# Kernel tuning notes

Hardware: AMD Instinct MI355X
Metric: run time of the kernel (lower is better)

The kernel has to match this reference:

```python
import jax, jax.numpy as jnp
import numpy as np

B, T, IN, H = 32, 256, 64, 128
TOP_K = 5
TRUNC = 100   # truncate_length: detach h,c every TRUNC steps
EPS = 1e-7
NEG = -1e9


def setup_inputs() -> dict:
    key = jax.random.key(0)
    ks = jax.random.split(key, 6)
    s = 1.0 / np.sqrt(H)  # torch LSTMCell default init bound
    xav = float(1.414 * np.sqrt(6.0 / (2 * H + 1)))  # xavier_uniform gain=1.414
    return {
        "x": jax.random.normal(ks[0], (B, T, IN), jnp.float32),
        "W_ih": jax.random.uniform(ks[1], (4 * H, IN), jnp.float32, -s, s),
        "W_hh": jax.random.uniform(ks[2], (4 * H, H), jnp.float32, -s, s),
        "b_ih": jax.random.uniform(ks[3], (4 * H,), jnp.float32, -s, s),
        "b_hh": jax.random.uniform(ks[4], (4 * H,), jnp.float32, -s, s),
        "w_t": jax.random.uniform(ks[5], (2 * H, 1), jnp.float32, -xav, xav),
    }


def _lstm_cell(x_t, h, c, W_ih, W_hh, b_ih, b_hh):
    # torch gate order: i, f, g, o
    g = x_t @ W_ih.T + h @ W_hh.T + (b_ih + b_hh)
    i, f, gg, o = jnp.split(g, 4, axis=-1)
    c = jax.nn.sigmoid(f) * c + jax.nn.sigmoid(i) * jnp.tanh(gg)
    h = jax.nn.sigmoid(o) * jnp.tanh(c)
    return h, c


def reference(x, W_ih, W_hh, b_ih, b_hh, w_t):
    Bv, Tv, _ = x.shape
    Hh = W_hh.shape[1]
    # score = w_t . tanh(cat(h_t, h_old)) splits additively since tanh is elementwise
    w_a = w_t[:Hh, 0]
    w_b = w_t[Hh:, 0]
    pos = jnp.arange(Tv + 1)

    def step(carry, inp):
        h, c, h_old = carry          # h_old: [B, T+1, H], slot 0 = initial zeros
        i, x_t = inp
        det = ((i + 1) % TRUNC) == 0
        h = jnp.where(det, jax.lax.stop_gradient(h), h)
        c = jnp.where(det, jax.lax.stop_gradient(c), c)
        h, c = _lstm_cell(x_t, h, c, W_ih, W_hh, b_ih, b_hh)
        rem = i + 1                  # remember_size
        mask = pos < rem             # [T+1] valid memory slots
        # attention scores over stored states
        s = (jnp.tanh(h) @ w_a)[:, None] + jnp.tanh(h_old) @ w_b  # [B, T+1]
        s_valid = jnp.where(mask[None, :], s, NEG)
        delta = jax.lax.top_k(s_valid, TOP_K)[0][:, -1] + EPS
        w_sp = jnp.clip(s_valid - delta[:, None], 0.0)
        w_sp = w_sp / (w_sp.sum(axis=1, keepdims=True) + EPS)
        # Sparse_attention returns raw scores when remember_size <= top_k
        attn_w = jnp.where(rem <= TOP_K, s, w_sp)
        attn_c = jnp.einsum('bt,bth->bh', jnp.where(mask[None, :], attn_w, 0.0), h_old)
        h = h + attn_c
        h_old = jax.lax.dynamic_update_slice(h_old, h[:, None, :], (0, rem, 0))
        return (h, c, h_old), (attn_c, attn_w)

    h0 = jnp.zeros((Bv, Hh), x.dtype)
    c0 = jnp.zeros((Bv, Hh), x.dtype)
    buf0 = jnp.zeros((Bv, Tv + 1, Hh), x.dtype)
    xs = (jnp.arange(Tv), jnp.swapaxes(x, 0, 1))
    _, (attn_c_all, attn_w_all) = jax.lax.scan(step, (h0, c0, buf0), xs)
    # module returns last step's (attn_c, out_attn_w); final remember_size == T
    return attn_c_all[-1], attn_w_all[-1][:, :Tv, None]
```

## Files before the change

kernel.cpp:

```cpp
#include <hip/hip_runtime.h>
#include <math.h>

#define NEGF -1000000000.0f
#define EPSF 1e-7f


typedef float v4f __attribute__((ext_vector_type(4)));
#define FMA4(a, b, c) __builtin_elementwise_fma((a), (b), (c))

#define RAWBAR() asm volatile("s_waitcnt lgkmcnt(0)\n\ts_barrier" ::: "memory")

__device__ __forceinline__ float fsigmoid(float x) {
  return 1.0f / (1.0f + __expf(-x));
}
__device__ __forceinline__ float ftanh(float x) {
  return 1.0f - 2.0f / (1.0f + __expf(2.0f * x));
}

__device__ __forceinline__ float wave_allsum(float v) {
#if __has_builtin(__builtin_amdgcn_update_dpp) && __has_builtin(__builtin_amdgcn_readlane)
  float f = v;
#define DPPSTEP(ctrl, rmask) { \
    int t = __builtin_amdgcn_update_dpp(0, __builtin_bit_cast(int, f), \
                                        ctrl, rmask, 0xf, true); \
    f += __builtin_bit_cast(float, t); }
  DPPSTEP(0x111, 0xf)
  DPPSTEP(0x112, 0xf)
  DPPSTEP(0x114, 0xf)
  DPPSTEP(0x118, 0xf)
  DPPSTEP(0x142, 0xa)
  DPPSTEP(0x143, 0x8)
#undef DPPSTEP
  return __builtin_bit_cast(float,
      __builtin_amdgcn_readlane(__builtin_bit_cast(int, f), 63));
#else
  for (int off = 1; off < 64; off <<= 1) v += __shfl_xor(v, off, 64);
  return v;
#endif
}

__global__ __launch_bounds__(512) void xw_kernel(
    const float* __restrict__ x, const float* __restrict__ W_ih,
    const float* __restrict__ b_ih, const float* __restrict__ b_hh,
    float* __restrict__ xw)
{
  const int t0 = blockIdx.x * 32;
  const int b  = blockIdx.y;
  const int g  = threadIdx.x;

  __shared__ float sx[32 * 64];
  ((float4*)sx)[threadIdx.x] =
      ((const float4*)(x + (size_t)(b * 256 + t0) * 64))[threadIdx.x];

  const float4* wr = (const float4*)(W_ih + (size_t)g * 64);
  float4 w0 = wr[0],  w1 = wr[1],  w2 = wr[2],  w3 = wr[3],
         w4 = wr[4],  w5 = wr[5],  w6 = wr[6],  w7 = wr[7],
         w8 = wr[8],  w9 = wr[9],  w10 = wr[10], w11 = wr[11],
         w12 = wr[12], w13 = wr[13], w14 = wr[14], w15 = wr[15];
  const float bias = b_ih[g] + b_hh[g];
  __syncthreads();

  float* dst = xw + (size_t)(b * 256 + t0) * 512 + g;
  for (int tt = 0; tt < 32; ++tt) {
    const float4* xr = (const float4*)(sx + tt * 64);
    float a0 = 0.0f, a1 = 0.0f, a2 = 0.0f, a3 = 0.0f;
#define XSTEP(j) { float4 hv = xr[j]; \
    a0 = fmaf(w##j.x, hv.x, a0); a1 = fmaf(w##j.y, hv.y, a1); \
    a2 = fmaf(w##j.z, hv.z, a2); a3 = fmaf(w##j.w, hv.w, a3); }
    XSTEP(0) XSTEP(1) XSTEP(2) XSTEP(3) XSTEP(4) XSTEP(5) XSTEP(6) XSTEP(7)
    XSTEP(8) XSTEP(9) XSTEP(10) XSTEP(11) XSTEP(12) XSTEP(13) XSTEP(14) XSTEP(15)
#undef XSTEP
    dst[(size_t)tt * 512] = (a0 + a1) + (a2 + a3) + bias;
  }
}

__global__
__attribute__((amdgpu_flat_work_group_size(512, 512), amdgpu_waves_per_eu(2, 2)))
void lstm_attn(
    const float* __restrict__ xw, const float* __restrict__ W_hh,
    const float* __restrict__ w_t, float* __restrict__ out)
{
  const int b   = blockIdx.x;
  const int tid = threadIdx.x;
  const int l   = tid & 63;
  const int wid = tid >> 6;
  const int g2  = tid & 255;
  const int q   = tid >> 8;

  __shared__ float ho[257 * 128];
  __shared__ float sh_part[2 * 512];
  __shared__ float sh_d[8];
  __shared__ float sh_pa[2];
  __shared__ float sh_dn[2];

  const v4f* pA = (const v4f*)(W_hh + (size_t)g2 * 128 + (q << 6));
  const v4f* pB = (const v4f*)(W_hh + (size_t)(g2 + 256) * 128 + (q << 6));
  v4f wA0 = pA[0],  wA1 = pA[1],  wA2 = pA[2],  wA3 = pA[3],
      wA4 = pA[4],  wA5 = pA[5],  wA6 = pA[6],  wA7 = pA[7],
      wA8 = pA[8],  wA9 = pA[9],  wA10 = pA[10], wA11 = pA[11],
      wA12 = pA[12], wA13 = pA[13], wA14 = pA[14], wA15 = pA[15];
  v4f wB0 = pB[0],  wB1 = pB[1],  wB2 = pB[2],  wB3 = pB[3],
      wB4 = pB[4],  wB5 = pB[5],  wB6 = pB[6],  wB7 = pB[7],
      wB8 = pB[8],  wB9 = pB[9],  wB10 = pB[10], wB11 = pB[11],
      wB12 = pB[12], wB13 = pB[13], wB14 = pB[14], wB15 = pB[15];

  const int j = (wid << 6) + l;
  float cc = 0.0f;
  float wa = 0.0f, wb = 0.0f;
  float t5v0 = 0.0f, t5v1 = NEGF, t5v2 = NEGF, t5v3 = NEGF, t5v4 = NEGF;
  int   t5i0 = 0, t5i1 = 0, t5i2 = 0, t5i3 = 0;
  float gn0 = 0.0f, gn1 = 0.0f, gn2 = 0.0f, gn3 = 0.0f;
  int   ofs0 = 0, ofs1 = 0, ofs2 = 0, ofs3 = 0;

  if (wid < 2) {
    wa = w_t[j]; wb = w_t[128 + j];
    ho[j] = 0.0f;
    __builtin_amdgcn_s_setprio(1);
  }
  if (tid == 0) sh_d[0] = 0.0f;
  __syncthreads();

  const float* xwb = xw + (size_t)b * 256 * 512;
  float xcA = 0.0f, xcB = 0.0f;
  if (q == 0) { xcA = xwb[g2]; xcB = xwb[g2 + 256]; }

  for (int i = 0; i < 256; ++i) {
    const int rem = i + 1;

    v4f aA = {xcA, 0.0f, 0.0f, 0.0f};
    v4f aB = {xcB, 0.0f, 0.0f, 0.0f};
    if (q == 0 && i < 255) {
      const float* xn = xwb + (size_t)(i + 1) * 512;
      xcA = xn[g2]; xcB = xn[g2 + 256];
    }
    const v4f* hh4 = (const v4f*)(ho + i * 128 + (q << 6));
#define KS(k) { v4f hv = hh4[k]; \
    aA = FMA4(wA##k, hv, aA); aB = FMA4(wB##k, hv, aB); }
    KS(0) KS(1) KS(2) KS(3) KS(4) KS(5) KS(6) KS(7)
    KS(8) KS(9) KS(10) KS(11) KS(12) KS(13) KS(14) KS(15)
#undef KS
    {
      float* sp = sh_part + (q << 9) + g2;
      sp[0]   = (aA.x + aA.y) + (aA.z + aA.w);
      sp[256] = (aB.x + aB.y) + (aB.z + aB.w);
    }

    float hv0 = 0.0f, hv1 = 0.0f, hv2 = 0.0f, hv3 = 0.0f;
    if (wid < 2 && i >= 5) {
      hv0 = ho[ofs0]; hv1 = ho[ofs1]; hv2 = ho[ofs2]; hv3 = ho[ofs3];
    }
    RAWBAR();

    float hc = 0.0f, at = 0.0f;
    if (wid < 2) {
      const float* s0 = sh_part + j;
      float Pi = s0[0]   + s0[512];
      float Pf = s0[128] + s0[640];
      float Pg = s0[256] + s0[768];
      float Po = s0[384] + s0[896];
      cc = fsigmoid(Pf) * cc + fsigmoid(Pi) * ftanh(Pg);
      hc = fsigmoid(Po) * ftanh(cc);
    }
    if (i < 5) {
      if (wid < 2) {
        float pa = wave_allsum(ftanh(hc) * wa);
        if (l == 0) sh_pa[wid] = pa;
      }
      RAWBAR();
      if (wid < 2) {
        float a = sh_pa[0] + sh_pa[1];
        at = 0.0f;
        for (int t = 0; t <= i; ++t)
          at = fmaf(a + sh_d[t], ho[t * 128 + j], at);
      }
    } else if (wid < 2) {
      at = gn0 * hv0;
      at = fmaf(gn1, hv1, at);
      at = fmaf(gn2, hv2, at);
      at = fmaf(gn3, hv3, at);
    }
    if (wid < 2) {
      float hn = hc + at;
      ho[rem * 128 + j] = hn;
      float pdn = wave_allsum(ftanh(hn) * wb);
      if (l == 0) sh_dn[wid] = pdn;
      if (i == 255) {
        out[b * 128 + j] = at;
        if (wid == 0) {
          #pragma unroll
          for (int m = 0; m < 4; ++m) {
            int t = l + 64 * m;
            float val = 0.0f;
            if (t == t5i0) val = gn0;
            if (t == t5i1) val = gn1;
            if (t == t5i2) val = gn2;
            if (t == t5i3) val = gn3;
            out[4096 + b * 256 + t] = val;
          }
        }
      }
    }
    RAWBAR();

    if (wid < 2 && i < 255) {
      float dn = sh_dn[0] + sh_dn[1];
      if (wid == 0 && l == 0 && i < 4) sh_d[rem] = dn;
      float v = dn; int vi = rem;
      if (v > t5v0) { float tv = t5v0; int ti = t5i0; t5v0 = v; t5i0 = vi; v = tv; vi = ti; }
      if (v > t5v1) { float tv = t5v1; int ti = t5i1; t5v1 = v; t5i1 = vi; v = tv; vi = ti; }
      if (v > t5v2) { float tv = t5v2; int ti = t5i2; t5v2 = v; t5i2 = vi; v = tv; vi = ti; }
      if (v > t5v3) { float tv = t5v3; int ti = t5i3; t5v3 = v; t5i3 = vi; v = tv; vi = ti; }
      if (v > t5v4) { t5v4 = v; }
      float g0 = fmaxf(t5v0 - t5v4 - EPSF, 0.0f);
      float g1 = fmaxf(t5v1 - t5v4 - EPSF, 0.0f);
      float g2f = fmaxf(t5v2 - t5v4 - EPSF, 0.0f);
      float g3 = fmaxf(t5v3 - t5v4 - EPSF, 0.0f);
      float inv = 1.0f / (((g0 + g1) + (g2f + g3)) + EPSF);
      gn0 = g0 * inv; gn1 = g1 * inv; gn2 = g2f * inv; gn3 = g3 * inv;
      ofs0 = (t5i0 << 7) + j; ofs1 = (t5i1 << 7) + j;
      ofs2 = (t5i2 << 7) + j; ofs3 = (t5i3 << 7) + j;
    }
  }
}

extern "C" void kernel_launch(void* const* d_in, const int* in_sizes, int n_in,
                              void* d_out, int out_size, void* d_ws, size_t ws_size,
                              hipStream_t stream) {
  const float* x    = (const float*)d_in[0];
  const float* W_ih = (const float*)d_in[1];
  const float* W_hh = (const float*)d_in[2];
  const float* b_ih = (const float*)d_in[3];
  const float* b_hh = (const float*)d_in[4];
  const float* w_t  = (const float*)d_in[5];
  float* out = (float*)d_out;

  float* xw = (float*)d_ws;

  xw_kernel<<<dim3(8, 32), 512, 0, stream>>>(x, W_ih, b_ih, b_hh, xw);
  lstm_attn<<<dim3(32), 512, 0, stream>>>(xw, W_hh, w_t, out);
}
```

Baseline: 368.1 us.

## Replicate LSTM cell update in every wave to drop a barrier per step

Each of the 8 waves now computes the full 128-wide gate and attention update redundantly, two hidden units per lane, and writes its own private copy of h. This removes the second block barrier per timestep and the cross-wave partial-sum exchange through shared memory. Top-k hidden states are kept in registers instead of a 257-step shared-memory history, and the gate partials are double-buffered so a single barrier per step suffices. The cost is redundant transcendental math in all waves and more register pressure, and the wave priority boost is dropped.

```diff
diff --git a/kernel.cpp b/kernel.cpp
--- a/kernel.cpp
+++ b/kernel.cpp
@@ -87,11 +87,10 @@
   const int g2  = tid & 255;
   const int q   = tid >> 8;
 
-  __shared__ float ho[257 * 128];
-  __shared__ float sh_part[2 * 512];
+  __shared__ float hpriv[8][128];
+  __shared__ float sh_part[2][1024];
+  __shared__ float ho5[5 * 128];
   __shared__ float sh_d[8];
-  __shared__ float sh_pa[2];
-  __shared__ float sh_dn[2];
 
   const v4f* pA = (const v4f*)(W_hh + (size_t)g2 * 128 + (q << 6));
   const v4f* pB = (const v4f*)(W_hh + (size_t)(g2 + 256) * 128 + (q << 6));
@@ -104,19 +103,18 @@
       wB8 = pB[8],  wB9 = pB[9],  wB10 = pB[10], wB11 = pB[11],
       wB12 = pB[12], wB13 = pB[13], wB14 = pB[14], wB15 = pB[15];
 
-  const int j = (wid << 6) + l;
-  float cc = 0.0f;
-  float wa = 0.0f, wb = 0.0f;
+  const int j0 = 2 * l, j1 = 2 * l + 1;
+  float cc0 = 0.0f, cc1 = 0.0f;
+  const float wa0 = w_t[j0], wa1 = w_t[j1];
+  const float wb0 = w_t[128 + j0], wb1 = w_t[128 + j1];
   float t5v0 = 0.0f, t5v1 = NEGF, t5v2 = NEGF, t5v3 = NEGF, t5v4 = NEGF;
   int   t5i0 = 0, t5i1 = 0, t5i2 = 0, t5i3 = 0;
+  float h5a0 = 0.0f, h5a1 = 0.0f, h5a2 = 0.0f, h5a3 = 0.0f;
+  float h5b0 = 0.0f, h5b1 = 0.0f, h5b2 = 0.0f, h5b3 = 0.0f;
   float gn0 = 0.0f, gn1 = 0.0f, gn2 = 0.0f, gn3 = 0.0f;
-  int   ofs0 = 0, ofs1 = 0, ofs2 = 0, ofs3 = 0;
-
-  if (wid < 2) {
-    wa = w_t[j]; wb = w_t[128 + j];
-    ho[j] = 0.0f;
-    __builtin_amdgcn_s_setprio(1);
-  }
+
+  *(float2*)(&hpriv[wid][j0]) = make_float2(0.0f, 0.0f);
+  if (wid == 0) *(float2*)(ho5 + j0) = make_float2(0.0f, 0.0f);
   if (tid == 0) sh_d[0] = 0.0f;
   __syncthreads();
 
@@ -133,83 +131,91 @@
       const float* xn = xwb + (size_t)(i + 1) * 512;
       xcA = xn[g2]; xcB = xn[g2 + 256];
     }
-    const v4f* hh4 = (const v4f*)(ho + i * 128 + (q << 6));
+    const v4f* hh4 = (const v4f*)(&hpriv[wid][q << 6]);
 #define KS(k) { v4f hv = hh4[k]; \
     aA = FMA4(wA##k, hv, aA); aB = FMA4(wB##k, hv, aB); }
     KS(0) KS(1) KS(2) KS(3) KS(4) KS(5) KS(6) KS(7)
     KS(8) KS(9) KS(10) KS(11) KS(12) KS(13) KS(14) KS(15)
 #undef KS
     {
-      float* sp = sh_part + (q << 9) + g2;
+      float* sp = sh_part[i & 1] + (q << 9) + g2;
       sp[0]   = (aA.x + aA.y) + (aA.z + aA.w);
       sp[256] = (aB.x + aB.y) + (aB.z + aB.w);
     }
-
-    float hv0 = 0.0f, hv1 = 0.0f, hv2 = 0.0f, hv3 = 0.0f;
-    if (wid < 2 && i >= 5) {
-      hv0 = ho[ofs0]; hv1 = ho[ofs1]; hv2 = ho[ofs2]; hv3 = ho[ofs3];
-    }
     RAWBAR();
 
-    float hc = 0.0f, at = 0.0f;
-    if (wid < 2) {
-      const float* s0 = sh_part + j;
-      float Pi = s0[0]   + s0[512];
-      float Pf = s0[128] + s0[640];
-      float Pg = s0[256] + s0[768];
-      float Po = s0[384] + s0[896];
-      cc = fsigmoid(Pf) * cc + fsigmoid(Pi) * ftanh(Pg);
-      hc = fsigmoid(Po) * ftanh(cc);
-    }
-    if (i < 5) {
-      if (wid < 2) {
-        float pa = wave_allsum(ftanh(hc) * wa);
-        if (l == 0) sh_pa[wid] = pa;
+    const float* s0 = sh_part[i & 1];
+    float2 Pi0 = *(const float2*)(s0 + j0);
+    float2 Pi1 = *(const float2*)(s0 + 512 + j0);
+    float2 Pf0 = *(const float2*)(s0 + 128 + j0);
+    float2 Pf1 = *(const float2*)(s0 + 640 + j0);
+    float2 Pg0 = *(const float2*)(s0 + 256 + j0);
+    float2 Pg1 = *(const float2*)(s0 + 768 + j0);
+    float2 Po0 = *(const float2*)(s0 + 384 + j0);
+    float2 Po1 = *(const float2*)(s0 + 896 + j0);
+    float Pi_x = Pi0.x + Pi1.x, Pi_y = Pi0.y + Pi1.y;
+    float Pf_x = Pf0.x + Pf1.x, Pf_y = Pf0.y + Pf1.y;
+    float Pg_x = Pg0.x + Pg1.x, Pg_y = Pg0.y + Pg1.y;
+    float Po_x = Po0.x + Po1.x, Po_y = Po0.y + Po1.y;
+    cc0 = fsigmoid(Pf_x) * cc0 + fsigmoid(Pi_x) * ftanh(Pg_x);
+    cc1 = fsigmoid(Pf_y) * cc1 + fsigmoid(Pi_y) * ftanh(Pg_y);
+    float hc0 = fsigmoid(Po_x) * ftanh(cc0);
+    float hc1 = fsigmoid(Po_y) * ftanh(cc1);
+
+    float at0, at1;
+    if (i >= 5) {
+      at0 = gn0 * h5a0;            at1 = gn0 * h5b0;
+      at0 = fmaf(gn1, h5a1, at0);  at1 = fmaf(gn1, h5b1, at1);
+      at0 = fmaf(gn2, h5a2, at0);  at1 = fmaf(gn2, h5b2, at1);
+      at0 = fmaf(gn3, h5a3, at0);  at1 = fmaf(gn3, h5b3, at1);
+    } else {
+      float a = wave_allsum(ftanh(hc0) * wa0 + ftanh(hc1) * wa1);
+      at0 = 0.0f; at1 = 0.0f;
+      for (int t = 0; t <= i; ++t) {
+        float s = a + sh_d[t];
+        float2 hv = *(const float2*)(ho5 + t * 128 + j0);
+        at0 = fmaf(s, hv.x, at0);
+        at1 = fmaf(s, hv.y, at1);
       }
-      RAWBAR();
-      if (wid < 2) {
-        float a = sh_pa[0] + sh_pa[1];
-        at = 0.0f;
-        for (int t = 0; t <= i; ++t)
-          at = fmaf(a + sh_d[t], ho[t * 128 + j], at);
+    }
+    float hn0 = hc0 + at0, hn1 = hc1 + at1;
+    *(float2*)(&hpriv[wid][j0]) = make_float2(hn0, hn1);
+    if (wid == 0 && rem <= 4)
+      *(float2*)(ho5 + rem * 128 + j0) = make_float2(hn0, hn1);
+    if (i == 255 && wid == 0) {
+      out[b * 128 + j0] = at0; out[b * 128 + j1] = at1;
+      #pragma unroll
+      for (int m = 0; m < 4; ++m) {
+        int t = l + 64 * m;
+        float val = 0.0f;
+        if (t == t5i0) val = gn0;
+        if (t == t5i1) val = gn1;
+        if (t == t5i2) val = gn2;
+        if (t == t5i3) val = gn3;
+        out[4096 + b * 256 + t] = val;
       }
-    } else if (wid < 2) {
-      at = gn0 * hv0;
-      at = fmaf(gn1, hv1, at);
-      at = fmaf(gn2, hv2, at);
-      at = fmaf(gn3, hv3, at);
-    }
-    if (wid < 2) {
-      float hn = hc + at;
-      ho[rem * 128 + j] = hn;
-      float pdn = wave_allsum(ftanh(hn) * wb);
-      if (l == 0) sh_dn[wid] = pdn;
-      if (i == 255) {
-        out[b * 128 + j] = at;
-        if (wid == 0) {
-          #pragma unroll
-          for (int m = 0; m < 4; ++m) {
-            int t = l + 64 * m;
-            float val = 0.0f;
-            if (t == t5i0) val = gn0;
-            if (t == t5i1) val = gn1;
-            if (t == t5i2) val = gn2;
-            if (t == t5i3) val = gn3;
-            out[4096 + b * 256 + t] = val;
-          }
-        }
-      }
-    }
-    RAWBAR();
-
-    if (wid < 2 && i < 255) {
-      float dn = sh_dn[0] + sh_dn[1];
+    }
+
+    if (i < 255) {
+      float dn = wave_allsum(ftanh(hn0) * wb0 + ftanh(hn1) * wb1);
       if (wid == 0 && l == 0 && i < 4) sh_d[rem] = dn;
-      float v = dn; int vi = rem;
-      if (v > t5v0) { float tv = t5v0; int ti = t5i0; t5v0 = v; t5i0 = vi; v = tv; vi = ti; }
-      if (v > t5v1) { float tv = t5v1; int ti = t5i1; t5v1 = v; t5i1 = vi; v = tv; vi = ti; }
-      if (v > t5v2) { float tv = t5v2; int ti = t5i2; t5v2 = v; t5i2 = vi; v = tv; vi = ti; }
-      if (v > t5v3) { float tv = t5v3; int ti = t5i3; t5v3 = v; t5i3 = vi; v = tv; vi = ti; }
+      float v = dn; int vi = rem; float va = hn0, vb = hn1;
+      if (v > t5v0) { float tv = t5v0; t5v0 = v; v = tv;
+                      int   ti = t5i0; t5i0 = vi; vi = ti;
+                      float ta = h5a0; h5a0 = va; va = ta;
+                      float tb = h5b0; h5b0 = vb; vb = tb; }
+      if (v > t5v1) { float tv = t5v1; t5v1 = v; v = tv;
+                      int   ti = t5i1; t5i1 = vi; vi = ti;
+                      float ta = h5a1; h5a1 = va; va = ta;
+                      float tb = h5b1; h5b1 = vb; vb = tb; }
+      if (v > t5v2) { float tv = t5v2; t5v2 = v; v = tv;
+                      int   ti = t5i2; t5i2 = vi; vi = ti;
+                      float ta = h5a2; h5a2 = va; va = ta;
+                      float tb = h5b2; h5b2 = vb; vb = tb; }
+      if (v > t5v3) { float tv = t5v3; t5v3 = v; v = tv;
+                      int   ti = t5i3; t5i3 = vi; vi = ti;
+                      float ta = h5a3; h5a3 = va; va = ta;
+                      float tb = h5b3; h5b3 = vb; vb = tb; }
       if (v > t5v4) { t5v4 = v; }
       float g0 = fmaxf(t5v0 - t5v4 - EPSF, 0.0f);
       float g1 = fmaxf(t5v1 - t5v4 - EPSF, 0.0f);
@@ -217,8 +223,6 @@
       float g3 = fmaxf(t5v3 - t5v4 - EPSF, 0.0f);
       float inv = 1.0f / (((g0 + g1) + (g2f + g3)) + EPSF);
       gn0 = g0 * inv; gn1 = g1 * inv; gn2 = g2f * inv; gn3 = g3 * inv;
-      ofs0 = (t5i0 << 7) + j; ofs1 = (t5i1 << 7) + j;
-      ofs2 = (t5i2 << 7) + j; ofs3 = (t5i3 << 7) + j;
     }
   }
 }
```

Result: slower. 526.1 us (+42.9%).

## Add two dedicated cell/attention waves separate from matvec waves

Applied to the files above, without the earlier changes.

Grows the recurrent block from 512 to 640 threads. The 8 original waves now only compute the W_hh matvec partials. Two extra waves (wid>=8) handle the LSTM cell update, the attention, the top-k tracking and the output writes. This splits the serial cell and attention work off the waves that hold the weight registers, aiming to relieve register pressure and scheduling contention. In exchange it adds more waves per CU and more threads taking part in every barrier. The 640-thread waves also load the weight registers they no longer use.

```diff
diff --git a/kernel.cpp b/kernel.cpp
--- a/kernel.cpp
+++ b/kernel.cpp
@@ -75,7 +75,7 @@
 }
 
 __global__
-__attribute__((amdgpu_flat_work_group_size(512, 512), amdgpu_waves_per_eu(2, 2)))
+__attribute__((amdgpu_flat_work_group_size(640, 640), amdgpu_waves_per_eu(2)))
 void lstm_attn(
     const float* __restrict__ xw, const float* __restrict__ W_hh,
     const float* __restrict__ w_t, float* __restrict__ out)
@@ -85,7 +85,8 @@
   const int l   = tid & 63;
   const int wid = tid >> 6;
   const int g2  = tid & 255;
-  const int q   = tid >> 8;
+  const int q   = (tid >> 8) & 1;
+  const int cw  = wid - 8;
 
   __shared__ float ho[257 * 128];
   __shared__ float sh_part[2 * 512];
@@ -104,7 +105,7 @@
       wB8 = pB[8],  wB9 = pB[9],  wB10 = pB[10], wB11 = pB[11],
       wB12 = pB[12], wB13 = pB[13], wB14 = pB[14], wB15 = pB[15];
 
-  const int j = (wid << 6) + l;
+  const int j = (cw << 6) + l;
   float cc = 0.0f;
   float wa = 0.0f, wb = 0.0f;
   float t5v0 = 0.0f, t5v1 = NEGF, t5v2 = NEGF, t5v3 = NEGF, t5v4 = NEGF;
@@ -112,7 +113,7 @@
   float gn0 = 0.0f, gn1 = 0.0f, gn2 = 0.0f, gn3 = 0.0f;
   int   ofs0 = 0, ofs1 = 0, ofs2 = 0, ofs3 = 0;
 
-  if (wid < 2) {
+  if (wid >= 8) {
     wa = w_t[j]; wb = w_t[128 + j];
     ho[j] = 0.0f;
     __builtin_amdgcn_s_setprio(1);
@@ -122,37 +123,37 @@
 
   const float* xwb = xw + (size_t)b * 256 * 512;
   float xcA = 0.0f, xcB = 0.0f;
-  if (q == 0) { xcA = xwb[g2]; xcB = xwb[g2 + 256]; }
+  if (wid < 8 && q == 0 && wid < 4) { xcA = xwb[g2]; xcB = xwb[g2 + 256]; }
 
   for (int i = 0; i < 256; ++i) {
     const int rem = i + 1;
 
-    v4f aA = {xcA, 0.0f, 0.0f, 0.0f};
-    v4f aB = {xcB, 0.0f, 0.0f, 0.0f};
-    if (q == 0 && i < 255) {
-      const float* xn = xwb + (size_t)(i + 1) * 512;
-      xcA = xn[g2]; xcB = xn[g2 + 256];
-    }
-    const v4f* hh4 = (const v4f*)(ho + i * 128 + (q << 6));
+    if (wid < 8) {
+      v4f aA = {xcA, 0.0f, 0.0f, 0.0f};
+      v4f aB = {xcB, 0.0f, 0.0f, 0.0f};
+      if (wid < 4 && i < 255) {
+        const float* xn = xwb + (size_t)(i + 1) * 512;
+        xcA = xn[g2]; xcB = xn[g2 + 256];
+      }
+      const v4f* hh4 = (const v4f*)(ho + i * 128 + (q << 6));
 #define KS(k) { v4f hv = hh4[k]; \
-    aA = FMA4(wA##k, hv, aA); aB = FMA4(wB##k, hv, aB); }
-    KS(0) KS(1) KS(2) KS(3) KS(4) KS(5) KS(6) KS(7)
-    KS(8) KS(9) KS(10) KS(11) KS(12) KS(13) KS(14) KS(15)
+      aA = FMA4(wA##k, hv, aA); aB = FMA4(wB##k, hv, aB); }
+      KS(0) KS(1) KS(2) KS(3) KS(4) KS(5) KS(6) KS(7)
+      KS(8) KS(9) KS(10) KS(11) KS(12) KS(13) KS(14) KS(15)
 #undef KS
-    {
       float* sp = sh_part + (q << 9) + g2;
       sp[0]   = (aA.x + aA.y) + (aA.z + aA.w);
       sp[256] = (aB.x + aB.y) + (aB.z + aB.w);
     }
 
     float hv0 = 0.0f, hv1 = 0.0f, hv2 = 0.0f, hv3 = 0.0f;
-    if (wid < 2 && i >= 5) {
+    if (wid >= 8 && i >= 5) {
       hv0 = ho[ofs0]; hv1 = ho[ofs1]; hv2 = ho[ofs2]; hv3 = ho[ofs3];
     }
     RAWBAR();
 
     float hc = 0.0f, at = 0.0f;
-    if (wid < 2) {
+    if (wid >= 8) {
       const float* s0 = sh_part + j;
       float Pi = s0[0]   + s0[512];
       float Pf = s0[128] + s0[640];
@@ -162,31 +163,32 @@
       hc = fsigmoid(Po) * ftanh(cc);
     }
     if (i < 5) {
-      if (wid < 2) {
+      if (wid >= 8) {
         float pa = wave_allsum(ftanh(hc) * wa);
-        if (l == 0) sh_pa[wid] = pa;
+        if (l == 0) sh_pa[cw] = pa;
       }
       RAWBAR();
-      if (wid < 2) {
+      if (wid >= 8) {
         float a = sh_pa[0] + sh_pa[1];
         at = 0.0f;
         for (int t = 0; t <= i; ++t)
           at = fmaf(a + sh_d[t], ho[t * 128 + j], at);
       }
-    } else if (wid < 2) {
+    } else if (wid >= 8) {
       at = gn0 * hv0;
       at = fmaf(gn1, hv1, at);
       at = fmaf(gn2, hv2, at);
       at = fmaf(gn3, hv3, at);
     }
-    if (wid < 2) {
-      float hn = hc + at;
+    float hn = 0.0f;
+    if (wid >= 8) {
+      hn = hc + at;
       ho[rem * 128 + j] = hn;
       float pdn = wave_allsum(ftanh(hn) * wb);
-      if (l == 0) sh_dn[wid] = pdn;
+      if (l == 0) sh_dn[cw] = pdn;
       if (i == 255) {
         out[b * 128 + j] = at;
-        if (wid == 0) {
+        if (cw == 0) {
           #pragma unroll
           for (int m = 0; m < 4; ++m) {
             int t = l + 64 * m;
@@ -202,9 +204,9 @@
     }
     RAWBAR();
 
-    if (wid < 2 && i < 255) {
+    if (wid >= 8 && i < 255) {
       float dn = sh_dn[0] + sh_dn[1];
-      if (wid == 0 && l == 0 && i < 4) sh_d[rem] = dn;
+      if (cw == 0 && l == 0 && i < 4) sh_d[rem] = dn;
       float v = dn; int vi = rem;
       if (v > t5v0) { float tv = t5v0; int ti = t5i0; t5v0 = v; t5i0 = vi; v = tv; vi = ti; }
       if (v > t5v1) { float tv = t5v1; int ti = t5i1; t5v1 = v; t5i1 = vi; v = tv; vi = ti; }
@@ -237,5 +239,5 @@
   float* xw = (float*)d_ws;
 
   xw_kernel<<<dim3(8, 32), 512, 0, stream>>>(x, W_ih, b_ih, b_hh, xw);
-  lstm_attn<<<dim3(32), 512, 0, stream>>>(xw, W_hh, w_t, out);
-}
+  lstm_attn<<<dim3(32), 640, 0, stream>>>(xw, W_hh, w_t, out);
+}
```

New measurement: 676.2 us. 1.84x slower.
